# Performance work log

Hardware: AMD Instinct MI355X
Metric: run time of the kernel (lower is better)

## Reference

```python
import math
import jax, jax.numpy as jnp
import numpy as np

B, FEAT, H, W = 4, 256, 48, 48
NH = 8
PE = 10            # pe_dim -> 3*PE = 30 positional channels
DK = FEAT // NH    # 32
DV = FEAT // NH    # 32
SCALE = 2.0 * math.pi
TEMPERATURE = 10000.0
BN_EPS = 1e-5


def pos_en_sine(h, w, num_pos_feats=PE):
    """3-axis sine positional encoding (y, x, and a constant 'o' axis) -> [3*PE, h, w]."""
    eps = 1e-6
    ones = jnp.ones((h, w), jnp.float32)
    y_embed = jnp.cumsum(ones, axis=0)
    x_embed = jnp.cumsum(ones, axis=1)
    y_embed = y_embed / (y_embed[-1:, :] + eps) * SCALE
    x_embed = x_embed / (x_embed[:, -1:] + eps) * SCALE
    o_embed = ones * SCALE  # third axis, constant when no explicit pos is given
    dim_t = jnp.arange(num_pos_feats, dtype=jnp.float32)
    dim_t = TEMPERATURE ** (2.0 * jnp.floor(dim_t / 2.0) / num_pos_feats)

    def enc(e):  # e: [h, w] -> [h, w, PE] interleaved sin/cos
        p = e[..., None] / dim_t
        return jnp.stack([jnp.sin(p[..., 0::2]), jnp.cos(p[..., 1::2])], axis=-1).reshape(h, w, num_pos_feats)

    pe = jnp.concatenate([enc(y_embed), enc(x_embed), enc(o_embed)], axis=-1)  # [h, w, 3*PE]
    return jnp.transpose(pe, (2, 0, 1))  # [3*PE, h, w]


def conv1x1(w, x):  # w: [out_c, in_c], x: [b, in_c, h, w]
    return jnp.einsum('oc,bchw->bohw', w, x)


def setup_inputs() -> dict:
    key = jax.random.key(0)
    ks = jax.random.split(key, 16)
    s = 0.02
    return {
        'q': jax.random.normal(ks[0], (B, FEAT, H, W), jnp.float32),
        'k': jax.random.normal(ks[1], (B, FEAT, H, W), jnp.float32),
        'v': jax.random.normal(ks[2], (B, FEAT, H, W), jnp.float32),
        'wq': jax.random.normal(ks[3], (NH * DK, FEAT + 3 * PE), jnp.float32) * s,
        'wk': jax.random.normal(ks[4], (NH * DK, FEAT + 3 * PE), jnp.float32) * s,
        'wv': jax.random.normal(ks[5], (NH * DV, FEAT), jnp.float32) * s,
        'wfc': jax.random.normal(ks[6], (FEAT, NH * DV), jnp.float32) * s,
        'w1': jax.random.normal(ks[7], (FEAT, FEAT), jnp.float32) * s,
        'b1': jnp.zeros((FEAT,), jnp.float32),
        'w2': jax.random.normal(ks[8], (FEAT, FEAT), jnp.float32) * s,
        'b2': jnp.zeros((FEAT,), jnp.float32),
        'gamma': jnp.ones((FEAT,), jnp.float32),
        'beta': jnp.zeros((FEAT,), jnp.float32),
    }


def reference(q, k, v, wq, wk, wv, wfc, w1, b1, w2, b2, gamma, beta):
    b, c, h, w = q.shape
    n = h * w
    pe = pos_en_sine(h, w)                                # [3*PE, h, w]
    peb = jnp.broadcast_to(pe[None], (b,) + pe.shape)
    qc = jnp.concatenate([q, peb], axis=1)                # [b, FEAT+30, h, w]
    kc = jnp.concatenate([k, peb], axis=1)
    # multi-head softmax attention over all spatial tokens
    Q = conv1x1(wq, qc).reshape(b, NH, DK, n)             # [b, nh, dk, n]
    K = conv1x1(wk, kc).reshape(b, NH, DK, n)
    V = conv1x1(wv, v).reshape(b, NH, DV, n)
    scores = jnp.einsum('bhdn,bhdm->bhnm', Q, K) / jnp.sqrt(jnp.float32(DK))
    attn = jax.nn.softmax(scores, axis=-1)                # [b, nh, n, n]
    O = jnp.einsum('bhnm,bhdm->bhdn', attn, V).reshape(b, NH * DV, h, w)
    O = conv1x1(wfc, O)                                   # [b, FEAT, h, w]
    # pointwise FFN + residual
    h1 = jax.nn.relu(conv1x1(w1, O) + b1[None, :, None, None])
    h2 = conv1x1(w2, h1) + b2[None, :, None, None]
    out = O + h2
    # BatchNorm2d (training mode: batch statistics over (b, h, w), biased var)
    mean = jnp.mean(out, axis=(0, 2, 3), keepdims=True)
    var = jnp.var(out, axis=(0, 2, 3), keepdims=True)
    out = (out - mean) / jnp.sqrt(var + BN_EPS)
    out = out * gamma[None, :, None, None] + beta[None, :, None, None]
    return out
```

## Files before the change

### kernel.cpp

```cpp
#include <hip/hip_runtime.h>
#include <hip/hip_bf16.h>

#define NTOK 2304

typedef short  short8  __attribute__((ext_vector_type(8)));
typedef unsigned short ushort8v __attribute__((ext_vector_type(8)));
typedef float  f32x4   __attribute__((ext_vector_type(4)));

static __device__ __forceinline__ unsigned short f2bfu(float f){
  __hip_bfloat16 h = __float2bfloat16(f);
  union { __hip_bfloat16 h; unsigned short u; } cv; cv.h = h; return cv.u;
}

static __device__ __forceinline__ void plane32(unsigned &a, unsigned &b){
  asm("v_permlane32_swap_b32 %0, %1" : "+v"(a), "+v"(b));
}
static __device__ __forceinline__ void plane16(unsigned &a, unsigned &b){
  asm("v_permlane16_swap_b32 %0, %1" : "+v"(a), "+v"(b));
}
static __device__ __forceinline__ short8 xpose_p(f32x4 sa, f32x4 sb){
  unsigned x0, x1, y0, y1;
  asm("v_cvt_pk_bf16_f32 %0, %1, %2" : "=v"(x0) : "v"(sa[0]), "v"(sa[1]));
  asm("v_cvt_pk_bf16_f32 %0, %1, %2" : "=v"(x1) : "v"(sa[2]), "v"(sa[3]));
  asm("v_cvt_pk_bf16_f32 %0, %1, %2" : "=v"(y0) : "v"(sb[0]), "v"(sb[1]));
  asm("v_cvt_pk_bf16_f32 %0, %1, %2" : "=v"(y1) : "v"(sb[2]), "v"(sb[3]));
  plane32(x0, y0);
  plane32(x1, y1);
  plane16(x0, y0);
  plane16(x1, y1);
  union { unsigned u[4]; short8 s; } r;
  r.u[0] = x0; r.u[1] = x1; r.u[2] = y0; r.u[3] = y1;
  return r.s;
}


__global__ void trip_kernel(float* out, int n){
  int i = blockIdx.x*256 + threadIdx.x;
  if (i < n) out[i] = 1000.0f;
}

__global__ __launch_bounds__(256) void setup_kernel(
    const float* __restrict__ q, const float* __restrict__ k,
    const float* __restrict__ v,
    const float* __restrict__ wq, const float* __restrict__ wk,
    const float* __restrict__ wv, const float* __restrict__ wfc,
    const float* __restrict__ w1, const float* __restrict__ w2,
    unsigned short* __restrict__ qT, unsigned short* __restrict__ kT,
    unsigned short* __restrict__ vT,
    unsigned short* __restrict__ wqp, unsigned short* __restrict__ wkp,
    unsigned short* __restrict__ wvb, unsigned short* __restrict__ wfcb,
    unsigned short* __restrict__ w1b, unsigned short* __restrict__ w2b,
    float* __restrict__ bns){
  const int bid = blockIdx.x;
  const int t = threadIdx.x;
  __shared__ __align__(16) unsigned short tile[64*72];

  if (bid < 1728){
    if (bid == 0){ bns[t] = 0.f; bns[256+t] = 0.f; }
    const int x = bid % 36, rem = bid / 36;
    const int y = rem % 4, z = rem / 4;
    const int tz = z >> 2, b = z & 3;
    const float* src = (tz==0) ? q : ((tz==1) ? k : v);
    unsigned short* dst = (tz==0) ? qT : ((tz==1) ? kT : vT);
    const int W = (tz==2) ? 256 : 288;
    const int n0 = x*64, c0 = y*64;
    const int jj = t & 7, cl = t >> 3;
    #pragma unroll
    for (int p=0; p<2; p++){
      int c = c0 + 32*p + cl;
      const float* s = src + (size_t)(b*256 + c)*NTOK + n0 + 8*jj;
      float4 f0 = *(const float4*)s;
      float4 f1 = *(const float4*)(s + 4);
      unsigned short* tr = tile + 32*p + cl;
      tr[(8*jj+0)*72] = f2bfu(f0.x); tr[(8*jj+1)*72] = f2bfu(f0.y);
      tr[(8*jj+2)*72] = f2bfu(f0.z); tr[(8*jj+3)*72] = f2bfu(f0.w);
      tr[(8*jj+4)*72] = f2bfu(f1.x); tr[(8*jj+5)*72] = f2bfu(f1.y);
      tr[(8*jj+6)*72] = f2bfu(f1.z); tr[(8*jj+7)*72] = f2bfu(f1.w);
    }
    __syncthreads();
    #pragma unroll
    for (int p=0; p<2; p++){
      int nl = 32*p + cl;
      ushort8v val = *(const ushort8v*)(tile + nl*72 + 8*jj);
      *(ushort8v*)(dst + (size_t)(b*2304 + n0 + nl)*W + c0 + 8*jj) = val;
    }
  } else if (bid < 1800){
    const int id2 = bid - 1728;
    const int x = id2 % 9, yy = id2 / 9;
    const int n = x*256 + t;
    unsigned short* buf = (yy < 4) ? qT : kT;
    const int b = yy & 3;
    const int i = n / 48, j = n - 48*i;
    const float k2pi = 6.283185307179586f;
    const float f = k2pi / 48.000001f;
    float ey = (float)(i+1) * f;
    float ex = (float)(j+1) * f;
    unsigned short u[32];
    #pragma unroll
    for (int p=0; p<10; p++){
      float inv = exp2f(-2.6575424759098898f * (float)(p >> 1));
      float vy = ey*inv, vx = ex*inv, vo = k2pi*inv;
      u[p]    = f2bfu((p&1) ? cosf(vy) : sinf(vy));
      u[10+p] = f2bfu((p&1) ? cosf(vx) : sinf(vx));
      u[20+p] = f2bfu((p&1) ? cosf(vo) : sinf(vo));
    }
    u[30] = 0; u[31] = 0;
    unsigned short* dst = buf + (size_t)(b*2304 + n)*288 + 256;
    #pragma unroll
    for (int m=0; m<4; m++) *(ushort8v*)(dst + 8*m) = *(const ushort8v*)(u + 8*m);
  } else if (bid < 2376){
    const int id3 = bid - 1800;
    const int x = id3 % 288, y = id3 / 288;
    const int idx = x*256 + t;
    const float* src = y ? wk : wq;
    unsigned short* dst = y ? wkp : wqp;
    const float scale = y ? 1.f : 0.25503486f;
    int row = idx / 288, col = idx - row*288;
    dst[idx] = (col < 286) ? f2bfu(src[row*286 + col] * scale) : (unsigned short)0;
  } else {
    const int id4 = bid - 2376;
    const int x = id4 % 256, y = id4 / 256;
    const int idx = x*256 + t;
    const float* src = (y==0)?wv:((y==1)?wfc:((y==2)?w1:w2));
    unsigned short* dst = (y==0)?wvb:((y==1)?wfcb:((y==2)?w1b:w2b));
    dst[idx] = f2bfu(src[idx]);
  }
}

template<int KSTEPS>
static __device__ __forceinline__ void gemm_core(
    const unsigned short* __restrict__ arow,
    const unsigned short* __restrict__ wrow, int wstride, f32x4* acc){
  #pragma unroll
  for (int kk=0; kk<KSTEPS; kk++){
    short8 af = *(const short8*)(arow + 32*kk);
    #pragma unroll
    for (int to=0; to<2; to++){
      short8 bf = *(const short8*)(wrow + (size_t)(16*to)*wstride + 32*kk);
      acc[to] = __builtin_amdgcn_mfma_f32_16x16x32_bf16(af, bf, acc[to], 0,0,0);
    }
  }
}

static __device__ __forceinline__ void epi_tok(
    const f32x4* acc, unsigned short* __restrict__ out_tok,
    int b, int tok, int n0, int lane, int quad, int cc,
    unsigned short* __restrict__ tlw){
  #pragma unroll
  for (int to=0; to<2; to++)
    #pragma unroll
    for (int r=0; r<4; r++)
      tlw[(4*quad + r)*40 + 16*to + cc] = f2bfu(acc[to][r]);
  const int row = lane & 15, ch = lane >> 4;
  ushort8v val = *(const ushort8v*)(tlw + row*40 + 8*ch);
  *(ushort8v*)(out_tok + (size_t)(b*2304 + tok + row)*256 + n0 + 8*ch) = val;
}

static __device__ __forceinline__ void epi_chan(
    const f32x4* acc, unsigned short* __restrict__ out_chan,
    int b, int tok, int n0, int quad, int cc){
  #pragma unroll
  for (int to=0; to<2; to++){
    ushort4 pk;
    pk.x = f2bfu(acc[to][0]); pk.y = f2bfu(acc[to][1]);
    pk.z = f2bfu(acc[to][2]); pk.w = f2bfu(acc[to][3]);
    *(ushort4*)(out_chan + (size_t)(b*256 + n0 + 16*to + cc)*NTOK + tok + 4*quad) = pk;
  }
}

__global__ __launch_bounds__(256) void qkv_kernel(
    const unsigned short* __restrict__ qT, const unsigned short* __restrict__ kT,
    const unsigned short* __restrict__ vT,
    const unsigned short* __restrict__ wqp, const unsigned short* __restrict__ wkp,
    const unsigned short* __restrict__ wvb,
    unsigned short* __restrict__ Qt, unsigned short* __restrict__ Kt,
    unsigned short* __restrict__ V2){
  const int t = threadIdx.x;
  const int w = t >> 6, lane = t & 63;
  const int quad = lane >> 4, cc = lane & 15;
  const int t0 = blockIdx.x*64, n0 = blockIdx.y*32;
  const int tz = blockIdx.z >> 2, b = blockIdx.z & 3;
  const int tok = t0 + 16*w;
  __shared__ __align__(16) unsigned short tl[4*16*40];
  unsigned short* tlw = tl + w*640;

  f32x4 acc[2];
  acc[0] = (f32x4){0.f,0.f,0.f,0.f}; acc[1] = acc[0];

  if (tz == 0){
    const unsigned short* arow = qT + (size_t)(b*2304 + tok + cc)*288 + 8*quad;
    const unsigned short* wrow = wqp + (size_t)(n0 + cc)*288 + 8*quad;
    gemm_core<9>(arow, wrow, 288, acc);
    epi_tok(acc, Qt, b, tok, n0, lane, quad, cc, tlw);
  } else if (tz == 1){
    const unsigned short* arow = kT + (size_t)(b*2304 + tok + cc)*288 + 8*quad;
    const unsigned short* wrow = wkp + (size_t)(n0 + cc)*288 + 8*quad;
    gemm_core<9>(arow, wrow, 288, acc);
    epi_tok(acc, Kt, b, tok, n0, lane, quad, cc, tlw);
  } else {
    const unsigned short* arow = vT + (size_t)(b*2304 + tok + cc)*256 + 8*quad;
    const unsigned short* wrow = wvb + (size_t)(n0 + cc)*256 + 8*quad;
    gemm_core<8>(arow, wrow, 256, acc);
    epi_chan(acc, V2, b, tok, n0, quad, cc);
  }
}

__global__ __launch_bounds__(256) void ffn_kernel(
    const unsigned short* __restrict__ AO,
    const unsigned short* __restrict__ wfcb,
    const unsigned short* __restrict__ w1b,
    const unsigned short* __restrict__ w2b,
    const float* __restrict__ b1, const float* __restrict__ b2,
    float* __restrict__ pre_out, float* __restrict__ bns){
  const int t = threadIdx.x;
  const int w = t >> 6, lane = t & 63;
  const int quad = lane >> 4, cc = lane & 15;
  const int tok0 = blockIdx.x * 16;
  const int b = blockIdx.y;
  const int ocb = 64 * w;

  __shared__ __align__(16) unsigned short T0[16*264];
  __shared__ __align__(16) unsigned short T1[16*264];

  const unsigned short* arow = AO + (size_t)(b*2304 + tok0 + cc)*256 + 8*quad;
  f32x4 acc1[4];
  acc1[0] = (f32x4){0.f,0.f,0.f,0.f}; acc1[1]=acc1[0]; acc1[2]=acc1[0]; acc1[3]=acc1[0];
  #pragma unroll
  for (int kk=0; kk<8; kk++){
    short8 af = *(const short8*)(arow + 32*kk);
    #pragma unroll
    for (int of=0; of<4; of++){
      short8 bf = *(const short8*)(wfcb + (size_t)(ocb + 16*of + cc)*256 + 8*quad + 32*kk);
      acc1[of] = __builtin_amdgcn_mfma_f32_16x16x32_bf16(af, bf, acc1[of], 0,0,0);
    }
  }
  #pragma unroll
  for (int of=0; of<4; of++)
    #pragma unroll
    for (int r=0; r<4; r++)
      T0[(4*quad + r)*264 + ocb + 16*of + cc] = f2bfu(acc1[of][r]);
  __syncthreads();

  f32x4 acc2[4];
  acc2[0] = (f32x4){0.f,0.f,0.f,0.f}; acc2[1]=acc2[0]; acc2[2]=acc2[0]; acc2[3]=acc2[0];
  #pragma unroll
  for (int kk=0; kk<8; kk++){
    short8 af = *(const short8*)(T0 + cc*264 + 8*quad + 32*kk);
    #pragma unroll
    for (int of=0; of<4; of++){
      short8 bf = *(const short8*)(w1b + (size_t)(ocb + 16*of + cc)*256 + 8*quad + 32*kk);
      acc2[of] = __builtin_amdgcn_mfma_f32_16x16x32_bf16(af, bf, acc2[of], 0,0,0);
    }
  }
  #pragma unroll
  for (int of=0; of<4; of++){
    float bv = b1[ocb + 16*of + cc];
    #pragma unroll
    for (int r=0; r<4; r++){
      float hv = fmaxf(acc2[of][r] + bv, 0.f);
      T1[(4*quad + r)*264 + ocb + 16*of + cc] = f2bfu(hv);
    }
  }
  __syncthreads();

  f32x4 acc3[4];
  acc3[0] = (f32x4){0.f,0.f,0.f,0.f}; acc3[1]=acc3[0]; acc3[2]=acc3[0]; acc3[3]=acc3[0];
  #pragma unroll
  for (int kk=0; kk<8; kk++){
    short8 af = *(const short8*)(T1 + cc*264 + 8*quad + 32*kk);
    #pragma unroll
    for (int of=0; of<4; of++){
      short8 bf = *(const short8*)(w2b + (size_t)(ocb + 16*of + cc)*256 + 8*quad + 32*kk);
      acc3[of] = __builtin_amdgcn_mfma_f32_16x16x32_bf16(af, bf, acc3[of], 0,0,0);
    }
  }
  #pragma unroll
  for (int of=0; of<4; of++){
    const int oc = ocb + 16*of + cc;
    float bv = b2[oc];
    float p0 = acc3[of][0] + bv + acc1[of][0];
    float p1 = acc3[of][1] + bv + acc1[of][1];
    float p2 = acc3[of][2] + bv + acc1[of][2];
    float p3 = acc3[of][3] + bv + acc1[of][3];
    *(float4*)(pre_out + (size_t)(b*256 + oc)*NTOK + tok0 + 4*quad) =
        make_float4(p0, p1, p2, p3);
    float s1 = (p0+p1)+(p2+p3);
    float s2 = (p0*p0+p1*p1)+(p2*p2+p3*p3);
    s1 += __shfl_xor(s1, 16, 64); s1 += __shfl_xor(s1, 32, 64);
    s2 += __shfl_xor(s2, 16, 64); s2 += __shfl_xor(s2, 32, 64);
    if (quad == 0){
      atomicAdd(&bns[oc],       s1);
      atomicAdd(&bns[256 + oc], s2);
    }
  }
}

__global__ __launch_bounds__(256) void attn_kernel(
    const unsigned short* __restrict__ Qt, const unsigned short* __restrict__ Kt,
    const unsigned short* __restrict__ V2, unsigned short* __restrict__ AO){
  const int t = threadIdx.x;
  const int w = t >> 6, lane = t & 63;
  const int quad = lane >> 4, cc = lane & 15;
  const int h = blockIdx.y, b = blockIdx.z;
  const int q0 = blockIdx.x*64;

  const unsigned short* qb = Qt + (size_t)(b*2304 + q0 + cc)*256 + h*32 + 8*quad;
  short8 qf0 = *(const short8*)(qb);
  short8 qf1 = *(const short8*)(qb + 16*256);
  short8 qf2 = *(const short8*)(qb + 32*256);
  short8 qf3 = *(const short8*)(qb + 48*256);

  const unsigned short* kb = Kt + (size_t)(b*2304 + cc)*256 + h*32 + 8*quad;
  const unsigned short* vb = V2 + (size_t)(b*256 + h*32 + cc)*NTOK + 8*quad;

  __shared__ __align__(16) float mg_lds[4*2112];

  f32x4 o00={0.f,0.f,0.f,0.f}, o10=o00, o01=o00, o11=o00;
  f32x4 o02=o00, o12=o00, o03=o00, o13=o00;
  float lsum0=0.f, lsum1=0.f, lsum2=0.f, lsum3=0.f;

  const int kstart = w*576;
  short8 kf0 = *(const short8*)(kb + (size_t)kstart*256);
  short8 kf1 = *(const short8*)(kb + (size_t)(kstart+16)*256);
  short8 vf0 = *(const short8*)(vb + kstart);
  short8 vf1 = *(const short8*)(vb + (size_t)16*NTOK + kstart);

  #pragma unroll 1
  for (int it = 0; it < 18; ++it){
    const int ko = kstart + it*32;
    const int rk = (it < 17) ? ko + 32 : kstart;
    const f32x4 z = {0.f,0.f,0.f,0.f};

    f32x4 s00 = __builtin_amdgcn_mfma_f32_16x16x32_bf16(kf0, qf0, z, 0,0,0);
    f32x4 s10 = __builtin_amdgcn_mfma_f32_16x16x32_bf16(kf1, qf0, z, 0,0,0);
    f32x4 s01 = __builtin_amdgcn_mfma_f32_16x16x32_bf16(kf0, qf1, z, 0,0,0);
    f32x4 s11 = __builtin_amdgcn_mfma_f32_16x16x32_bf16(kf1, qf1, z, 0,0,0);
    f32x4 s02 = __builtin_amdgcn_mfma_f32_16x16x32_bf16(kf0, qf2, z, 0,0,0);
    f32x4 s12 = __builtin_amdgcn_mfma_f32_16x16x32_bf16(kf1, qf2, z, 0,0,0);
    f32x4 s03 = __builtin_amdgcn_mfma_f32_16x16x32_bf16(kf0, qf3, z, 0,0,0);
    f32x4 s13 = __builtin_amdgcn_mfma_f32_16x16x32_bf16(kf1, qf3, z, 0,0,0);
    kf0 = *(const short8*)(kb + (size_t)rk*256);
    kf1 = *(const short8*)(kb + (size_t)(rk+16)*256);

    #pragma unroll
    for (int r=0; r<4; r++){
      s00[r] = __builtin_amdgcn_exp2f(s00[r]);
      s10[r] = __builtin_amdgcn_exp2f(s10[r]);
      s01[r] = __builtin_amdgcn_exp2f(s01[r]);
      s11[r] = __builtin_amdgcn_exp2f(s11[r]);
      s02[r] = __builtin_amdgcn_exp2f(s02[r]);
      s12[r] = __builtin_amdgcn_exp2f(s12[r]);
      s03[r] = __builtin_amdgcn_exp2f(s03[r]);
      s13[r] = __builtin_amdgcn_exp2f(s13[r]);
    }
    lsum0 += ((s00[0]+s00[1])+(s00[2]+s00[3])) + ((s10[0]+s10[1])+(s10[2]+s10[3]));
    lsum1 += ((s01[0]+s01[1])+(s01[2]+s01[3])) + ((s11[0]+s11[1])+(s11[2]+s11[3]));
    lsum2 += ((s02[0]+s02[1])+(s02[2]+s02[3])) + ((s12[0]+s12[1])+(s12[2]+s12[3]));
    lsum3 += ((s03[0]+s03[1])+(s03[2]+s03[3])) + ((s13[0]+s13[1])+(s13[2]+s13[3]));

    short8 pf0 = xpose_p(s00, s10);
    short8 pf1 = xpose_p(s01, s11);
    short8 pf2 = xpose_p(s02, s12);
    short8 pf3 = xpose_p(s03, s13);

    o00 = __builtin_amdgcn_mfma_f32_16x16x32_bf16(vf0, pf0, o00, 0,0,0);
    o10 = __builtin_amdgcn_mfma_f32_16x16x32_bf16(vf1, pf0, o10, 0,0,0);
    o01 = __builtin_amdgcn_mfma_f32_16x16x32_bf16(vf0, pf1, o01, 0,0,0);
    o11 = __builtin_amdgcn_mfma_f32_16x16x32_bf16(vf1, pf1, o11, 0,0,0);
    o02 = __builtin_amdgcn_mfma_f32_16x16x32_bf16(vf0, pf2, o02, 0,0,0);
    o12 = __builtin_amdgcn_mfma_f32_16x16x32_bf16(vf1, pf2, o12, 0,0,0);
    o03 = __builtin_amdgcn_mfma_f32_16x16x32_bf16(vf0, pf3, o03, 0,0,0);
    o13 = __builtin_amdgcn_mfma_f32_16x16x32_bf16(vf1, pf3, o13, 0,0,0);
    vf0 = *(const short8*)(vb + rk);
    vf1 = *(const short8*)(vb + (size_t)16*NTOK + rk);
  }

  lsum0 += __shfl_xor(lsum0, 16, 64); lsum0 += __shfl_xor(lsum0, 32, 64);
  lsum1 += __shfl_xor(lsum1, 16, 64); lsum1 += __shfl_xor(lsum1, 32, 64);
  lsum2 += __shfl_xor(lsum2, 16, 64); lsum2 += __shfl_xor(lsum2, 32, 64);
  lsum3 += __shfl_xor(lsum3, 16, 64); lsum3 += __shfl_xor(lsum3, 32, 64);

  float* mg = mg_lds + w*2112;
  #pragma unroll
  for (int i=0;i<4;i++){
    mg[(0*8 + 0*4 + i)*64 + lane] = o00[i];
    mg[(0*8 + 1*4 + i)*64 + lane] = o10[i];
    mg[(1*8 + 0*4 + i)*64 + lane] = o01[i];
    mg[(1*8 + 1*4 + i)*64 + lane] = o11[i];
    mg[(2*8 + 0*4 + i)*64 + lane] = o02[i];
    mg[(2*8 + 1*4 + i)*64 + lane] = o12[i];
    mg[(3*8 + 0*4 + i)*64 + lane] = o03[i];
    mg[(3*8 + 1*4 + i)*64 + lane] = o13[i];
  }
  if (quad == 0){
    mg[2048 +  0 + cc] = lsum0;
    mg[2048 + 16 + cc] = lsum1;
    mg[2048 + 32 + cc] = lsum2;
    mg[2048 + 48 + cc] = lsum3;
  }
  __syncthreads();

  const float* m0 = mg_lds;
  const float* m1 = mg_lds + 2112;
  const float* m2 = mg_lds + 4224;
  const float* m3 = mg_lds + 6336;
  const int la = 2048 + w*16 + cc;
  float ls = (m0[la] + m1[la]) + (m2[la] + m3[la]);
  float inv = 1.f / ls;

  float r0, r1, r2, r3, r4, r5, r6, r7;
  {
    int a0 = (w*8 + 0)*64 + lane;
    r0 = (m0[a0] + m1[a0]) + (m2[a0] + m3[a0]);
    int a1 = (w*8 + 1)*64 + lane;
    r1 = (m0[a1] + m1[a1]) + (m2[a1] + m3[a1]);
    int a2 = (w*8 + 2)*64 + lane;
    r2 = (m0[a2] + m1[a2]) + (m2[a2] + m3[a2]);
    int a3 = (w*8 + 3)*64 + lane;
    r3 = (m0[a3] + m1[a3]) + (m2[a3] + m3[a3]);
    int a4 = (w*8 + 4)*64 + lane;
    r4 = (m0[a4] + m1[a4]) + (m2[a4] + m3[a4]);
    int a5 = (w*8 + 5)*64 + lane;
    r5 = (m0[a5] + m1[a5]) + (m2[a5] + m3[a5]);
    int a6 = (w*8 + 6)*64 + lane;
    r6 = (m0[a6] + m1[a6]) + (m2[a6] + m3[a6]);
    int a7 = (w*8 + 7)*64 + lane;
    r7 = (m0[a7] + m1[a7]) + (m2[a7] + m3[a7]);
  }

  const int qcol = q0 + w*16 + cc;
  unsigned short* dst = AO + (size_t)(b*2304 + qcol)*256 + h*32 + 4*quad;
  ushort4 p0;
  p0.x = f2bfu(r0*inv); p0.y = f2bfu(r1*inv);
  p0.z = f2bfu(r2*inv); p0.w = f2bfu(r3*inv);
  *(ushort4*)(dst) = p0;
  ushort4 p1;
  p1.x = f2bfu(r4*inv); p1.y = f2bfu(r5*inv);
  p1.z = f2bfu(r6*inv); p1.w = f2bfu(r7*inv);
  *(ushort4*)(dst + 16) = p1;
}

__global__ __launch_bounds__(256) void bn_final_kernel(
    const float* __restrict__ pre, const float* __restrict__ bns,
    const float* __restrict__ g, const float* __restrict__ bt,
    float* __restrict__ out){
  int i0 = (blockIdx.x*256 + threadIdx.x)*4;
  int ch = (i0 / NTOK) & 255;
  float mean = bns[ch] * (1.f/9216.f);
  float var  = bns[256+ch] * (1.f/9216.f) - mean*mean;
  float scl = g[ch] * rsqrtf(fmaxf(var, 0.f) + 1e-5f);
  float sh  = bt[ch] - mean*scl;
  float4 x = *(const float4*)(pre + i0);
  *(float4*)(out + i0) = make_float4(x.x*scl+sh, x.y*scl+sh, x.z*scl+sh, x.w*scl+sh);
}

extern "C" void kernel_launch(void* const* d_in, const int* in_sizes, int n_in,
                              void* d_out, int out_size, void* d_ws, size_t ws_size,
                              hipStream_t stream){
  const size_t NEED = 2112 + (size_t)15155200*2;
  if (ws_size < NEED){
    trip_kernel<<<dim3((out_size+255)/256), dim3(256), 0, stream>>>((float*)d_out, out_size);
    return;
  }
  const float* q   = (const float*)d_in[0];
  const float* k   = (const float*)d_in[1];
  const float* v   = (const float*)d_in[2];
  const float* wq  = (const float*)d_in[3];
  const float* wk  = (const float*)d_in[4];
  const float* wv  = (const float*)d_in[5];
  const float* wfc = (const float*)d_in[6];
  const float* w1  = (const float*)d_in[7];
  const float* b1  = (const float*)d_in[8];
  const float* w2  = (const float*)d_in[9];
  const float* b2  = (const float*)d_in[10];
  const float* gm  = (const float*)d_in[11];
  const float* bt  = (const float*)d_in[12];

  float* ws  = (float*)d_ws;
  float* bns = ws;
  unsigned short* ub = (unsigned short*)(ws + 528);
  unsigned short* u_qT = ub;
  unsigned short* u_kT = ub + 2654208;
  unsigned short* u_vT = ub + 5308416;
  unsigned short* u_Qt = ub + 7667712;
  unsigned short* u_Kt = ub + 10027008;
  unsigned short* u_V2 = ub + 12386304;
  unsigned short* wqp  = ub + 14745600;
  unsigned short* wkp  = ub + 14819328;
  unsigned short* wvb  = ub + 14893056;
  unsigned short* wfcb = ub + 14958592;
  unsigned short* w1b  = ub + 15024128;
  unsigned short* w2b  = ub + 15089664;
  unsigned short* AO  = u_qT;
  float* pre = (float*)(u_Kt);

  setup_kernel<<<dim3(3400), dim3(256), 0, stream>>>(
      q, k, v, wq, wk, wv, wfc, w1, w2,
      u_qT, u_kT, u_vT, wqp, wkp, wvb, wfcb, w1b, w2b, bns);

  qkv_kernel<<<dim3(36,8,12), dim3(256), 0, stream>>>(u_qT, u_kT, u_vT, wqp, wkp, wvb, u_Qt, u_Kt, u_V2);

  attn_kernel<<<dim3(36,8,4), dim3(256), 0, stream>>>(u_Qt, u_Kt, u_V2, AO);

  ffn_kernel<<<dim3(144,4), dim3(256), 0, stream>>>(AO, wfcb, w1b, w2b, b1, b2, pre, bns);

  bn_final_kernel<<<dim3(2304), dim3(256), 0, stream>>>(pre, bns, gm, bt, (float*)d_out);
}
```

Baseline: 230.6 us.

## Compute three token tiles per wave in QKV GEMM and trim attention merge LDS

The QKV projection kernel now has each wave compute three 16-token tiles instead of one, reusing every weight fragment load across three MFMAs, and the grid shrinks threefold to match. The attention kernel's cross-wave merge now skips writing each wave's own partial to LDS and keeps it in registers, so the LDS buffer and read traffic get smaller. Risks are higher register pressure and fewer blocks in the QKV kernel (1152 instead of 3456), which may reduce latency hiding.

```diff
diff --git a/kernel.cpp b/kernel.cpp
--- a/kernel.cpp
+++ b/kernel.cpp
@@ -128,16 +128,22 @@
 }
 
 template<int KSTEPS>
-static __device__ __forceinline__ void gemm_core(
-    const unsigned short* __restrict__ arow,
-    const unsigned short* __restrict__ wrow, int wstride, f32x4* acc){
+static __device__ __forceinline__ void gemm3_core(
+    const unsigned short* __restrict__ a0,
+    const unsigned short* __restrict__ a1,
+    const unsigned short* __restrict__ a2,
+    const unsigned short* __restrict__ wrow, int wstride, f32x4 acc[3][2]){
   #pragma unroll
   for (int kk=0; kk<KSTEPS; kk++){
-    short8 af = *(const short8*)(arow + 32*kk);
+    short8 af0 = *(const short8*)(a0 + 32*kk);
+    short8 af1 = *(const short8*)(a1 + 32*kk);
+    short8 af2 = *(const short8*)(a2 + 32*kk);
     #pragma unroll
     for (int to=0; to<2; to++){
       short8 bf = *(const short8*)(wrow + (size_t)(16*to)*wstride + 32*kk);
-      acc[to] = __builtin_amdgcn_mfma_f32_16x16x32_bf16(af, bf, acc[to], 0,0,0);
+      acc[0][to] = __builtin_amdgcn_mfma_f32_16x16x32_bf16(af0, bf, acc[0][to], 0,0,0);
+      acc[1][to] = __builtin_amdgcn_mfma_f32_16x16x32_bf16(af1, bf, acc[1][to], 0,0,0);
+      acc[2][to] = __builtin_amdgcn_mfma_f32_16x16x32_bf16(af2, bf, acc[2][to], 0,0,0);
     }
   }
 }
@@ -178,30 +184,40 @@
   const int t = threadIdx.x;
   const int w = t >> 6, lane = t & 63;
   const int quad = lane >> 4, cc = lane & 15;
-  const int t0 = blockIdx.x*64, n0 = blockIdx.y*32;
+  const int t0 = blockIdx.x*192, n0 = blockIdx.y*32;
   const int tz = blockIdx.z >> 2, b = blockIdx.z & 3;
-  const int tok = t0 + 16*w;
+  const int tok = t0 + 48*w;
   __shared__ __align__(16) unsigned short tl[4*16*40];
   unsigned short* tlw = tl + w*640;
 
-  f32x4 acc[2];
-  acc[0] = (f32x4){0.f,0.f,0.f,0.f}; acc[1] = acc[0];
+  f32x4 acc[3][2];
+  #pragma unroll
+  for (int f=0; f<3; f++){
+    acc[f][0] = (f32x4){0.f,0.f,0.f,0.f};
+    acc[f][1] = acc[f][0];
+  }
 
   if (tz == 0){
-    const unsigned short* arow = qT + (size_t)(b*2304 + tok + cc)*288 + 8*quad;
-    const unsigned short* wrow = wqp + (size_t)(n0 + cc)*288 + 8*quad;
-    gemm_core<9>(arow, wrow, 288, acc);
-    epi_tok(acc, Qt, b, tok, n0, lane, quad, cc, tlw);
+    const unsigned short* a0 = qT + (size_t)(b*2304 + tok + cc)*288 + 8*quad;
+    gemm3_core<9>(a0, a0 + (size_t)16*288, a0 + (size_t)32*288,
+                  wqp + (size_t)(n0 + cc)*288 + 8*quad, 288, acc);
+    epi_tok(acc[0], Qt, b, tok,      n0, lane, quad, cc, tlw);
+    epi_tok(acc[1], Qt, b, tok + 16, n0, lane, quad, cc, tlw);
+    epi_tok(acc[2], Qt, b, tok + 32, n0, lane, quad, cc, tlw);
   } else if (tz == 1){
-    const unsigned short* arow = kT + (size_t)(b*2304 + tok + cc)*288 + 8*quad;
-    const unsigned short* wrow = wkp + (size_t)(n0 + cc)*288 + 8*quad;
-    gemm_core<9>(arow, wrow, 288, acc);
-    epi_tok(acc, Kt, b, tok, n0, lane, quad, cc, tlw);
+    const unsigned short* a0 = kT + (size_t)(b*2304 + tok + cc)*288 + 8*quad;
+    gemm3_core<9>(a0, a0 + (size_t)16*288, a0 + (size_t)32*288,
+                  wkp + (size_t)(n0 + cc)*288 + 8*quad, 288, acc);
+    epi_tok(acc[0], Kt, b, tok,      n0, lane, quad, cc, tlw);
+    epi_tok(acc[1], Kt, b, tok + 16, n0, lane, quad, cc, tlw);
+    epi_tok(acc[2], Kt, b, tok + 32, n0, lane, quad, cc, tlw);
   } else {
-    const unsigned short* arow = vT + (size_t)(b*2304 + tok + cc)*256 + 8*quad;
-    const unsigned short* wrow = wvb + (size_t)(n0 + cc)*256 + 8*quad;
-    gemm_core<8>(arow, wrow, 256, acc);
-    epi_chan(acc, V2, b, tok, n0, quad, cc);
+    const unsigned short* a0 = vT + (size_t)(b*2304 + tok + cc)*256 + 8*quad;
+    gemm3_core<8>(a0, a0 + (size_t)16*256, a0 + (size_t)32*256,
+                  wvb + (size_t)(n0 + cc)*256 + 8*quad, 256, acc);
+    epi_chan(acc[0], V2, b, tok,      n0, quad, cc);
+    epi_chan(acc[1], V2, b, tok + 16, n0, quad, cc);
+    epi_chan(acc[2], V2, b, tok + 32, n0, quad, cc);
   }
 }
 
@@ -313,7 +329,7 @@
   const unsigned short* kb = Kt + (size_t)(b*2304 + cc)*256 + h*32 + 8*quad;
   const unsigned short* vb = V2 + (size_t)(b*256 + h*32 + cc)*NTOK + 8*quad;
 
-  __shared__ __align__(16) float mg_lds[4*2112];
+  __shared__ __align__(16) float mg_lds[4*1600];
 
   f32x4 o00={0.f,0.f,0.f,0.f}, o10=o00, o01=o00, o11=o00;
   f32x4 o02=o00, o12=o00, o03=o00, o13=o00;
@@ -380,63 +396,59 @@
   lsum2 += __shfl_xor(lsum2, 16, 64); lsum2 += __shfl_xor(lsum2, 32, 64);
   lsum3 += __shfl_xor(lsum3, 16, 64); lsum3 += __shfl_xor(lsum3, 32, 64);
 
-  float* mg = mg_lds + w*2112;
-  #pragma unroll
-  for (int i=0;i<4;i++){
-    mg[(0*8 + 0*4 + i)*64 + lane] = o00[i];
-    mg[(0*8 + 1*4 + i)*64 + lane] = o10[i];
-    mg[(1*8 + 0*4 + i)*64 + lane] = o01[i];
-    mg[(1*8 + 1*4 + i)*64 + lane] = o11[i];
-    mg[(2*8 + 0*4 + i)*64 + lane] = o02[i];
-    mg[(2*8 + 1*4 + i)*64 + lane] = o12[i];
-    mg[(3*8 + 0*4 + i)*64 + lane] = o03[i];
-    mg[(3*8 + 1*4 + i)*64 + lane] = o13[i];
+  float* mg = mg_lds + w*1600;
+  #pragma unroll
+  for (int qq=0; qq<4; qq++){
+    f32x4 a0, a1;
+    if (qq==0){ a0=o00; a1=o10; }
+    else if (qq==1){ a0=o01; a1=o11; }
+    else if (qq==2){ a0=o02; a1=o12; }
+    else { a0=o03; a1=o13; }
+    if (qq != w){
+      const int p = (qq < w) ? qq : qq - 1;
+      #pragma unroll
+      for (int i=0;i<4;i++){
+        mg[(p*8 + i)*64 + lane]     = a0[i];
+        mg[(p*8 + 4 + i)*64 + lane] = a1[i];
+      }
+    }
   }
   if (quad == 0){
-    mg[2048 +  0 + cc] = lsum0;
-    mg[2048 + 16 + cc] = lsum1;
-    mg[2048 + 32 + cc] = lsum2;
-    mg[2048 + 48 + cc] = lsum3;
+    mg[1536 +  0 + cc] = lsum0;
+    mg[1536 + 16 + cc] = lsum1;
+    mg[1536 + 32 + cc] = lsum2;
+    mg[1536 + 48 + cc] = lsum3;
   }
   __syncthreads();
 
-  const float* m0 = mg_lds;
-  const float* m1 = mg_lds + 2112;
-  const float* m2 = mg_lds + 4224;
-  const float* m3 = mg_lds + 6336;
-  const int la = 2048 + w*16 + cc;
-  float ls = (m0[la] + m1[la]) + (m2[la] + m3[la]);
+  f32x4 R0, R1; float ls;
+  if (w==0){ R0=o00; R1=o10; ls=lsum0; }
+  else if (w==1){ R0=o01; R1=o11; ls=lsum1; }
+  else if (w==2){ R0=o02; R1=o12; ls=lsum2; }
+  else { R0=o03; R1=o13; ls=lsum3; }
+  #pragma unroll
+  for (int v=0; v<4; v++){
+    if (v == w) continue;
+    const float* m = mg_lds + v*1600;
+    const int p = (w < v) ? w : w - 1;
+    #pragma unroll
+    for (int i=0;i<4;i++){
+      R0[i] += m[(p*8 + i)*64 + lane];
+      R1[i] += m[(p*8 + 4 + i)*64 + lane];
+    }
+    ls += m[1536 + w*16 + cc];
+  }
   float inv = 1.f / ls;
-
-  float r0, r1, r2, r3, r4, r5, r6, r7;
-  {
-    int a0 = (w*8 + 0)*64 + lane;
-    r0 = (m0[a0] + m1[a0]) + (m2[a0] + m3[a0]);
-    int a1 = (w*8 + 1)*64 + lane;
-    r1 = (m0[a1] + m1[a1]) + (m2[a1] + m3[a1]);
-    int a2 = (w*8 + 2)*64 + lane;
-    r2 = (m0[a2] + m1[a2]) + (m2[a2] + m3[a2]);
-    int a3 = (w*8 + 3)*64 + lane;
-    r3 = (m0[a3] + m1[a3]) + (m2[a3] + m3[a3]);
-    int a4 = (w*8 + 4)*64 + lane;
-    r4 = (m0[a4] + m1[a4]) + (m2[a4] + m3[a4]);
-    int a5 = (w*8 + 5)*64 + lane;
-    r5 = (m0[a5] + m1[a5]) + (m2[a5] + m3[a5]);
-    int a6 = (w*8 + 6)*64 + lane;
-    r6 = (m0[a6] + m1[a6]) + (m2[a6] + m3[a6]);
-    int a7 = (w*8 + 7)*64 + lane;
-    r7 = (m0[a7] + m1[a7]) + (m2[a7] + m3[a7]);
-  }
 
   const int qcol = q0 + w*16 + cc;
   unsigned short* dst = AO + (size_t)(b*2304 + qcol)*256 + h*32 + 4*quad;
   ushort4 p0;
-  p0.x = f2bfu(r0*inv); p0.y = f2bfu(r1*inv);
-  p0.z = f2bfu(r2*inv); p0.w = f2bfu(r3*inv);
+  p0.x = f2bfu(R0[0]*inv); p0.y = f2bfu(R0[1]*inv);
+  p0.z = f2bfu(R0[2]*inv); p0.w = f2bfu(R0[3]*inv);
   *(ushort4*)(dst) = p0;
   ushort4 p1;
-  p1.x = f2bfu(r4*inv); p1.y = f2bfu(r5*inv);
-  p1.z = f2bfu(r6*inv); p1.w = f2bfu(r7*inv);
+  p1.x = f2bfu(R1[0]*inv); p1.y = f2bfu(R1[1]*inv);
+  p1.z = f2bfu(R1[2]*inv); p1.w = f2bfu(R1[3]*inv);
   *(ushort4*)(dst + 16) = p1;
 }
 
@@ -498,7 +510,7 @@
       q, k, v, wq, wk, wv, wfc, w1, w2,
       u_qT, u_kT, u_vT, wqp, wkp, wvb, wfcb, w1b, w2b, bns);
 
-  qkv_kernel<<<dim3(36,8,12), dim3(256), 0, stream>>>(u_qT, u_kT, u_vT, wqp, wkp, wvb, u_Qt, u_Kt, u_V2);
+  qkv_kernel<<<dim3(12,8,12), dim3(256), 0, stream>>>(u_qT, u_kT, u_vT, wqp, wkp, wvb, u_Qt, u_Kt, u_V2);
 
   attn_kernel<<<dim3(36,8,4), dim3(256), 0, stream>>>(u_Qt, u_Kt, u_V2, AO);
 
```

Result: faster. 220.8 us (median of 2 runs) (-4.3%).
